# Kernel tuning notes

Hardware: AMD Instinct MI355X
Metric: run time of the kernel (lower is better)

## Reference

```python
import jax, jax.numpy as jnp
import numpy as np

NEG_BIG = -9e15  # matches torch's -9000000000000000.0 mask value
ALPHA = 0.2      # LeakyReLU negative slope


def setup_inputs() -> dict:
    key = jax.random.key(0)
    k1, k2, k3 = jax.random.split(key, 3)
    B, N, Fin, Fout = 8, 2048, 64, 64
    h = jax.random.normal(k1, (B, N, Fin), dtype=jnp.float32)
    adj = jax.random.randint(k2, (B, N, N), 0, 2, dtype=jnp.int32)
    kW, ka = jax.random.split(k3)
    # xavier_uniform with gain=1.414
    gW = 1.414 * np.sqrt(6.0 / (Fin + Fout))
    W = jax.random.uniform(kW, (Fin, Fout), minval=-gW, maxval=gW, dtype=jnp.float32)
    ga = 1.414 * np.sqrt(6.0 / (2 * Fout + 1))
    a = jax.random.uniform(ka, (2 * Fout, 1), minval=-ga, maxval=ga, dtype=jnp.float32)
    return {"h": h, "adj": adj, "W": W, "a": a}


def reference(h, adj, W, a):
    # Wh: [B, N, Fout]
    Wh = jnp.einsum("bnf,fo->bno", h, W)
    Fout = W.shape[1]
    a1 = a[:Fout, 0]   # source part of attention vector
    a2 = a[Fout:, 0]   # target part
    # e_ij = leakyrelu(a1.Wh_i + a2.Wh_j) -- rank-1 decomposition of the
    # repeat/cat construction; avoids the [B,N,N,2F] intermediate.
    s = Wh @ a1        # [B, N]
    t = Wh @ a2        # [B, N]
    e = s[:, :, None] + t[:, None, :]            # [B, N, N]
    e = jnp.where(e > 0, e, ALPHA * e)           # LeakyReLU
    e = jnp.where(adj > 0, e, NEG_BIG)           # adjacency mask
    attention = jax.nn.softmax(e, axis=2)
    # dropout omitted: reference is eval-mode (F.dropout is identity when not training)
    h_prime = jnp.einsum("bij,bjo->bio", attention, Wh)
    return jax.nn.elu(h_prime)                   # concat=True branch
```

## Files before the change

### kernel.cpp

```cpp
#include <hip/hip_runtime.h>


#define ALPHA 0.2f

typedef __attribute__((ext_vector_type(8))) short  short8;
typedef __attribute__((ext_vector_type(4))) float  f32x4;

static __device__ __forceinline__ unsigned short f2bf(float f) {
    unsigned u = __builtin_bit_cast(unsigned, f);
    u += 0x7fffu + ((u >> 16) & 1u);
    return (unsigned short)(u >> 16);
}

static __device__ __forceinline__ unsigned pack_bf2(float lo, float hi) {
    unsigned ulo = __builtin_bit_cast(unsigned, lo) + 0x8000u;
    unsigned uhi = __builtin_bit_cast(unsigned, hi) + 0x8000u;
    return __builtin_amdgcn_perm(uhi, ulo, 0x07060302);
}

__global__ __launch_bounds__(256) void k01(
    const float* __restrict__ h, const int* __restrict__ adj,
    const float* __restrict__ W, const float* __restrict__ a,
    unsigned short* __restrict__ whT, float* __restrict__ sw,
    float* __restrict__ tw, unsigned char* __restrict__ mask)
{
    __shared__ float W_l[64 * 65];
    __shared__ float wa[128];
    __shared__ float tile[4 * 16 * 65];

    const int tid = threadIdx.x;

    if (blockIdx.x >= 256) {
        const int mb = blockIdx.x - 256;
        const int4* a4 = (const int4*)adj;
        #pragma unroll 1
        for (int g0 = 0; g0 < 16; g0 += 4) {
            int4 v0a, v0b, v1a, v1b, v2a, v2b, v3a, v3b;
            const size_t p0 = (size_t)mb * 4096 + (size_t)g0 * 256 + tid;
            v0a = a4[p0 * 2];          v0b = a4[p0 * 2 + 1];
            v1a = a4[(p0 + 256) * 2];  v1b = a4[(p0 + 256) * 2 + 1];
            v2a = a4[(p0 + 512) * 2];  v2b = a4[(p0 + 512) * 2 + 1];
            v3a = a4[(p0 + 768) * 2];  v3b = a4[(p0 + 768) * 2 + 1];
            unsigned b0 = (v0a.x ? 1u:0u)|(v0a.y ? 2u:0u)|(v0a.z ? 4u:0u)|(v0a.w ? 8u:0u)
                        | (v0b.x ?16u:0u)|(v0b.y ?32u:0u)|(v0b.z ?64u:0u)|(v0b.w ?128u:0u);
            unsigned b1 = (v1a.x ? 1u:0u)|(v1a.y ? 2u:0u)|(v1a.z ? 4u:0u)|(v1a.w ? 8u:0u)
                        | (v1b.x ?16u:0u)|(v1b.y ?32u:0u)|(v1b.z ?64u:0u)|(v1b.w ?128u:0u);
            unsigned b2 = (v2a.x ? 1u:0u)|(v2a.y ? 2u:0u)|(v2a.z ? 4u:0u)|(v2a.w ? 8u:0u)
                        | (v2b.x ?16u:0u)|(v2b.y ?32u:0u)|(v2b.z ?64u:0u)|(v2b.w ?128u:0u);
            unsigned b3 = (v3a.x ? 1u:0u)|(v3a.y ? 2u:0u)|(v3a.z ? 4u:0u)|(v3a.w ? 8u:0u)
                        | (v3b.x ?16u:0u)|(v3b.y ?32u:0u)|(v3b.z ?64u:0u)|(v3b.w ?128u:0u);
            mask[p0]       = (unsigned char)b0;
            mask[p0 + 256] = (unsigned char)b1;
            mask[p0 + 512] = (unsigned char)b2;
            mask[p0 + 768] = (unsigned char)b3;
        }
        return;
    }

    const int lane = tid & 63, wv = tid >> 6;
    const int im   = lane & 15, kq = lane >> 4;

    #pragma unroll
    for (int k = 0; k < 16; ++k) {
        int e = tid + 256 * k;
        W_l[(e >> 6) * 65 + (e & 63)] = W[e];
    }
    __syncthreads();

    if (tid < 128) {
        int f = tid & 63;
        const float* ap = a + (tid >> 6) * 64;
        float acc = 0.f;
        #pragma unroll 8
        for (int o = 0; o < 64; ++o) acc += W_l[f * 65 + o] * ap[o];
        wa[tid] = acc;
    }
    __syncthreads();

    short8 bf[4][2];
    #pragma unroll
    for (int nb = 0; nb < 4; ++nb)
        #pragma unroll
        for (int ks = 0; ks < 2; ++ks)
            #pragma unroll
            for (int u = 0; u < 8; ++u)
                bf[nb][ks][u] = (short)f2bf(W_l[(ks * 32 + kq * 8 + u) * 65 + nb * 16 + im]);

    const int row0 = blockIdx.x * 64 + wv * 16;
    const int bb = row0 >> 11, n_base = row0 & 2047;
    const float* hrow = h + (size_t)(row0 + im) * 64;

    float hv[2][8];
    short8 af[2];
    float sp = 0.f, tp = 0.f;
    #pragma unroll
    for (int ks = 0; ks < 2; ++ks) {
        float4 A = *(const float4*)(hrow + ks * 32 + kq * 8);
        float4 Bv = *(const float4*)(hrow + ks * 32 + kq * 8 + 4);
        hv[ks][0] = A.x;  hv[ks][1] = A.y;  hv[ks][2] = A.z;  hv[ks][3] = A.w;
        hv[ks][4] = Bv.x; hv[ks][5] = Bv.y; hv[ks][6] = Bv.z; hv[ks][7] = Bv.w;
        #pragma unroll
        for (int u = 0; u < 8; ++u) {
            int f = ks * 32 + kq * 8 + u;
            sp += hv[ks][u] * wa[f];
            tp += hv[ks][u] * wa[64 + f];
            af[ks][u] = (short)f2bf(hv[ks][u]);
        }
    }
    sp += __shfl_xor(sp, 16, 64); sp += __shfl_xor(sp, 32, 64);
    tp += __shfl_xor(tp, 16, 64); tp += __shfl_xor(tp, 32, 64);
    if (lane < 16) {
        sw[row0 + lane] = sp;
        tw[row0 + lane] = tp;
    }

    f32x4 acc[4] = {{0.f,0.f,0.f,0.f},{0.f,0.f,0.f,0.f},{0.f,0.f,0.f,0.f},{0.f,0.f,0.f,0.f}};
    #pragma unroll
    for (int ks = 0; ks < 2; ++ks)
        #pragma unroll
        for (int nb = 0; nb < 4; ++nb)
            acc[nb] = __builtin_amdgcn_mfma_f32_16x16x32_bf16(af[ks], bf[nb][ks], acc[nb], 0, 0, 0);

    #pragma unroll
    for (int nb = 0; nb < 4; ++nb)
        #pragma unroll
        for (int r = 0; r < 4; ++r)
            tile[wv * 1040 + (kq * 4 + r) * 65 + nb * 16 + im] = acc[nb][r];
    __syncthreads();

    #pragma unroll
    for (int k = 0; k < 16; ++k) {
        int o = kq + 4 * k;
        float v = tile[wv * 1040 + im * 65 + o];
        whT[(size_t)(bb * 64 + o) * 2048 + n_base + im] = f2bf(v);
    }
}

__global__ __launch_bounds__(256, 2) void k2_attn(
    const unsigned* __restrict__ mask, const unsigned short* __restrict__ whT,
    const float* __restrict__ sw, const float* __restrict__ tw,
    float* __restrict__ out)
{
    __shared__ float t_l[2048];
    __shared__ float cpart[4 * 1040];
    __shared__ float zp[64];

    const int tid  = threadIdx.x;
    const int lane = tid & 63, wv = tid >> 6;
    const int im   = lane & 15, kq = lane >> 4;
    const int b    = blockIdx.x >> 7;
    const int i0   = (blockIdx.x & 127) << 4;

    {
        const float4* tp4 = (const float4*)(tw + (size_t)b * 2048);
        *(float4*)&t_l[tid * 4]         = tp4[tid];
        *(float4*)&t_l[(tid + 256) * 4] = tp4[tid + 256];
    }

    const uint4* mrow4 = (const uint4*)(mask + (size_t)(b * 2048 + i0 + im) * 64 + wv * 16);
    const uint4 mA = mrow4[0], mB = mrow4[1], mC = mrow4[2], mD = mrow4[3];
    const unsigned mm[16] = {mA.x, mA.y, mA.z, mA.w, mB.x, mB.y, mB.z, mB.w,
                             mC.x, mC.y, mC.z, mC.w, mD.x, mD.y, mD.z, mD.w};

    const float sl = sw[b * 2048 + i0 + im];
    const int j00 = wv * 512 + kq * 8;
    const unsigned short* whp0 = whT + ((size_t)(b * 64 +  0 + im) * 2048 + j00);
    const unsigned short* whp1 = whT + ((size_t)(b * 64 + 16 + im) * 2048 + j00);
    const unsigned short* whp2 = whT + ((size_t)(b * 64 + 32 + im) * 2048 + j00);
    const unsigned short* whp3 = whT + ((size_t)(b * 64 + 48 + im) * 2048 + j00);

    __syncthreads();

    f32x4 acc0 = {0.f,0.f,0.f,0.f}, acc1 = {0.f,0.f,0.f,0.f};
    f32x4 acc2 = {0.f,0.f,0.f,0.f}, acc3 = {0.f,0.f,0.f,0.f};
    float zs = 0.f;

    #pragma unroll
    for (int s = 0; s < 16; ++s) {
        const short8 w0 = *(const short8*)(const void*)(whp0 + s * 32);
        const short8 w1 = *(const short8*)(const void*)(whp1 + s * 32);
        const short8 w2 = *(const short8*)(const void*)(whp2 + s * 32);
        const short8 w3 = *(const short8*)(const void*)(whp3 + s * 32);

        const float4 tA = *(const float4*)&t_l[j00 + s * 32];
        const float4 tB = *(const float4*)&t_l[j00 + s * 32 + 4];
        const unsigned mbyte = (mm[s] >> (kq * 8)) & 0xffu;

        float e0 = sl + tA.x; e0 = fmaxf(e0, ALPHA * e0);
        float e1 = sl + tA.y; e1 = fmaxf(e1, ALPHA * e1);
        float e2 = sl + tA.z; e2 = fmaxf(e2, ALPHA * e2);
        float e3 = sl + tA.w; e3 = fmaxf(e3, ALPHA * e3);
        float e4 = sl + tB.x; e4 = fmaxf(e4, ALPHA * e4);
        float e5 = sl + tB.y; e5 = fmaxf(e5, ALPHA * e5);
        float e6 = sl + tB.z; e6 = fmaxf(e6, ALPHA * e6);
        float e7 = sl + tB.w; e7 = fmaxf(e7, ALPHA * e7);

        float p0 = (mbyte &   1u) ? __expf(e0) : 0.f;
        float p1 = (mbyte &   2u) ? __expf(e1) : 0.f;
        float p2 = (mbyte &   4u) ? __expf(e2) : 0.f;
        float p3 = (mbyte &   8u) ? __expf(e3) : 0.f;
        float p4 = (mbyte &  16u) ? __expf(e4) : 0.f;
        float p5 = (mbyte &  32u) ? __expf(e5) : 0.f;
        float p6 = (mbyte &  64u) ? __expf(e6) : 0.f;
        float p7 = (mbyte & 128u) ? __expf(e7) : 0.f;

        zs += ((p0 + p1) + (p2 + p3)) + ((p4 + p5) + (p6 + p7));

        int4 ai;
        ai.x = (int)pack_bf2(p0, p1);
        ai.y = (int)pack_bf2(p2, p3);
        ai.z = (int)pack_bf2(p4, p5);
        ai.w = (int)pack_bf2(p6, p7);
        const short8 af = __builtin_bit_cast(short8, ai);

        acc0 = __builtin_amdgcn_mfma_f32_16x16x32_bf16(af, w0, acc0, 0, 0, 0);
        acc1 = __builtin_amdgcn_mfma_f32_16x16x32_bf16(af, w1, acc1, 0, 0, 0);
        acc2 = __builtin_amdgcn_mfma_f32_16x16x32_bf16(af, w2, acc2, 0, 0, 0);
        acc3 = __builtin_amdgcn_mfma_f32_16x16x32_bf16(af, w3, acc3, 0, 0, 0);
    }

    zs += __shfl_xor(zs, 16, 64);
    zs += __shfl_xor(zs, 32, 64);
    if (lane < 16) zp[wv * 16 + lane] = zs;

    #pragma unroll
    for (int r = 0; r < 4; ++r) {
        cpart[wv * 1040 + (kq * 4 + r) * 65 +  0 + im] = acc0[r];
        cpart[wv * 1040 + (kq * 4 + r) * 65 + 16 + im] = acc1[r];
        cpart[wv * 1040 + (kq * 4 + r) * 65 + 32 + im] = acc2[r];
        cpart[wv * 1040 + (kq * 4 + r) * 65 + 48 + im] = acc3[r];
    }
    __syncthreads();

    #pragma unroll
    for (int k = 0; k < 4; ++k) {
        int idx = tid + 256 * k;
        int i = idx >> 6, o = idx & 63;
        float ssum = cpart[0 * 1040 + i * 65 + o] + cpart[1 * 1040 + i * 65 + o]
                   + cpart[2 * 1040 + i * 65 + o] + cpart[3 * 1040 + i * 65 + o];
        float z = zp[i] + zp[16 + i] + zp[32 + i] + zp[48 + i];
        if (z == 0.f) z = 1.f;
        float r = ssum / z;
        out[((size_t)(b * 2048 + i0 + i)) * 64 + o] = r > 0.f ? r : expm1f(r);
    }
}

extern "C" void kernel_launch(void* const* d_in, const int* in_sizes, int n_in,
                              void* d_out, int out_size, void* d_ws, size_t ws_size,
                              hipStream_t stream) {
    const float* h   = (const float*)d_in[0];
    const int*   adj = (const int*)d_in[1];
    const float* W   = (const float*)d_in[2];
    const float* a   = (const float*)d_in[3];
    float* out = (float*)d_out;

    unsigned short* whT = (unsigned short*)d_ws;
    float* sw  = (float*)((char*)d_ws + 2097152);
    float* tw  = (float*)((char*)d_ws + 2097152 + 65536);
    unsigned char* mask = (unsigned char*)((char*)d_ws + 2097152 + 131072);

    hipLaunchKernelGGL(k01, dim3(1280), dim3(256), 0, stream, h, adj, W, a, whT, sw, tw, mask);
    hipLaunchKernelGGL(k2_attn, dim3(1024), dim3(256), 0, stream,
                       (const unsigned*)mask, whT, sw, tw, out);
}
```

Baseline: 233.0 us.

## Factor exp of LeakyReLU into per-row and per-column exps; pre-swizzle Wh fragments

The attention kernel no longer evaluates exp per (i,j) pair. It precomputes exp(t_j) and exp(alpha*t_j) per column and exp(s_i), exp(alpha*s_i) per row, then forms each weight as a product, picking a branch by whether exp(s+t) exceeds one. The first kernel now writes Wh in an MFMA-fragment-ordered layout, so each lane loads one contiguous 16-byte uint4 per B operand. This removes the per-element transcendental work and the strided global loads. The cost is extra LDS traffic, and the softmax has no max subtraction, so the exp products can overflow or underflow for large s or t.

Result: faster. 214.9 us (-7.7%).

```diff
diff --git a/kernel.cpp b/kernel.cpp
--- a/kernel.cpp
+++ b/kernel.cpp
@@ -21,7 +21,7 @@
 __global__ __launch_bounds__(256) void k01(
     const float* __restrict__ h, const int* __restrict__ adj,
     const float* __restrict__ W, const float* __restrict__ a,
-    unsigned short* __restrict__ whT, float* __restrict__ sw,
+    uint4* __restrict__ whF, float* __restrict__ sw,
     float* __restrict__ tw, unsigned char* __restrict__ mask)
 {
     __shared__ float W_l[64 * 65];
@@ -87,7 +87,6 @@
                 bf[nb][ks][u] = (short)f2bf(W_l[(ks * 32 + kq * 8 + u) * 65 + nb * 16 + im]);
 
     const int row0 = blockIdx.x * 64 + wv * 16;
-    const int bb = row0 >> 11, n_base = row0 & 2047;
     const float* hrow = h + (size_t)(row0 + im) * 64;
 
     float hv[2][8];
@@ -128,20 +127,44 @@
             tile[wv * 1040 + (kq * 4 + r) * 65 + nb * 16 + im] = acc[nb][r];
     __syncthreads();
 
-    #pragma unroll
-    for (int k = 0; k < 16; ++k) {
-        int o = kq + 4 * k;
-        float v = tile[wv * 1040 + im * 65 + o];
-        whT[(size_t)(bb * 64 + o) * 2048 + n_base + im] = f2bf(v);
+    {
+        const int blk_row0 = blockIdx.x * 64;
+        const int bb2 = blk_row0 >> 11;
+        const int c_base = (blk_row0 & 2047) >> 5;
+        #pragma unroll
+        for (int k = 0; k < 2; ++k) {
+            int e = tid + 256 * k;
+            int l = e & 63, ot = (e >> 6) & 3, cl_ = e >> 8;
+            int o = ot * 16 + (l & 15);
+            int jb = cl_ * 32 + (l >> 4) * 8;
+            unsigned d0, d1, d2, d3;
+            {
+                int j0 = jb;
+                d0 = pack_bf2(tile[(j0 >> 4) * 1040 + (j0 & 15) * 65 + o],
+                              tile[(j0 >> 4) * 1040 + ((j0 & 15) + 1) * 65 + o]);
+                j0 = jb + 2;
+                d1 = pack_bf2(tile[(j0 >> 4) * 1040 + (j0 & 15) * 65 + o],
+                              tile[(j0 >> 4) * 1040 + ((j0 & 15) + 1) * 65 + o]);
+                j0 = jb + 4;
+                d2 = pack_bf2(tile[(j0 >> 4) * 1040 + (j0 & 15) * 65 + o],
+                              tile[(j0 >> 4) * 1040 + ((j0 & 15) + 1) * 65 + o]);
+                j0 = jb + 6;
+                d3 = pack_bf2(tile[(j0 >> 4) * 1040 + (j0 & 15) * 65 + o],
+                              tile[(j0 >> 4) * 1040 + ((j0 & 15) + 1) * 65 + o]);
+            }
+            uint4 val = {d0, d1, d2, d3};
+            whF[(size_t)(((bb2 * 64 + c_base + cl_) * 4 + ot)) * 64 + l] = val;
+        }
     }
 }
 
 __global__ __launch_bounds__(256, 2) void k2_attn(
-    const unsigned* __restrict__ mask, const unsigned short* __restrict__ whT,
+    const unsigned* __restrict__ mask, const uint4* __restrict__ whF,
     const float* __restrict__ sw, const float* __restrict__ tw,
     float* __restrict__ out)
 {
-    __shared__ float t_l[2048];
+    __shared__ float eB[2048];
+    __shared__ float eD[2048];
     __shared__ float cpart[4 * 1040];
     __shared__ float zp[64];
 
@@ -153,8 +176,13 @@
 
     {
         const float4* tp4 = (const float4*)(tw + (size_t)b * 2048);
-        *(float4*)&t_l[tid * 4]         = tp4[tid];
-        *(float4*)&t_l[(tid + 256) * 4] = tp4[tid + 256];
+        float4 t0 = tp4[tid], t1 = tp4[tid + 256];
+        float4 e0 = {__expf(t0.x), __expf(t0.y), __expf(t0.z), __expf(t0.w)};
+        float4 e1 = {__expf(t1.x), __expf(t1.y), __expf(t1.z), __expf(t1.w)};
+        float4 f0 = {__expf(ALPHA*t0.x), __expf(ALPHA*t0.y), __expf(ALPHA*t0.z), __expf(ALPHA*t0.w)};
+        float4 f1 = {__expf(ALPHA*t1.x), __expf(ALPHA*t1.y), __expf(ALPHA*t1.z), __expf(ALPHA*t1.w)};
+        *(float4*)&eB[tid * 4] = e0;  *(float4*)&eB[(tid + 256) * 4] = e1;
+        *(float4*)&eD[tid * 4] = f0;  *(float4*)&eD[(tid + 256) * 4] = f1;
     }
 
     const uint4* mrow4 = (const uint4*)(mask + (size_t)(b * 2048 + i0 + im) * 64 + wv * 16);
@@ -163,11 +191,9 @@
                              mC.x, mC.y, mC.z, mC.w, mD.x, mD.y, mD.z, mD.w};
 
     const float sl = sw[b * 2048 + i0 + im];
+    const float al = __expf(sl), cl_ = __expf(ALPHA * sl);
     const int j00 = wv * 512 + kq * 8;
-    const unsigned short* whp0 = whT + ((size_t)(b * 64 +  0 + im) * 2048 + j00);
-    const unsigned short* whp1 = whT + ((size_t)(b * 64 + 16 + im) * 2048 + j00);
-    const unsigned short* whp2 = whT + ((size_t)(b * 64 + 32 + im) * 2048 + j00);
-    const unsigned short* whp3 = whT + ((size_t)(b * 64 + 48 + im) * 2048 + j00);
+    const uint4* wbase = whF + (size_t)((b * 64 + wv * 16) * 4) * 64 + lane;
 
     __syncthreads();
 
@@ -177,32 +203,34 @@
 
     #pragma unroll
     for (int s = 0; s < 16; ++s) {
-        const short8 w0 = *(const short8*)(const void*)(whp0 + s * 32);
-        const short8 w1 = *(const short8*)(const void*)(whp1 + s * 32);
-        const short8 w2 = *(const short8*)(const void*)(whp2 + s * 32);
-        const short8 w3 = *(const short8*)(const void*)(whp3 + s * 32);
-
-        const float4 tA = *(const float4*)&t_l[j00 + s * 32];
-        const float4 tB = *(const float4*)&t_l[j00 + s * 32 + 4];
+        const uint4 w0 = wbase[(s * 4 + 0) * 64];
+        const uint4 w1 = wbase[(s * 4 + 1) * 64];
+        const uint4 w2 = wbase[(s * 4 + 2) * 64];
+        const uint4 w3 = wbase[(s * 4 + 3) * 64];
+
+        const float4 bA = *(const float4*)&eB[j00 + s * 32];
+        const float4 bBv = *(const float4*)&eB[j00 + s * 32 + 4];
+        const float4 dA = *(const float4*)&eD[j00 + s * 32];
+        const float4 dBv = *(const float4*)&eD[j00 + s * 32 + 4];
         const unsigned mbyte = (mm[s] >> (kq * 8)) & 0xffu;
 
-        float e0 = sl + tA.x; e0 = fmaxf(e0, ALPHA * e0);
-        float e1 = sl + tA.y; e1 = fmaxf(e1, ALPHA * e1);
-        float e2 = sl + tA.z; e2 = fmaxf(e2, ALPHA * e2);
-        float e3 = sl + tA.w; e3 = fmaxf(e3, ALPHA * e3);
-        float e4 = sl + tB.x; e4 = fmaxf(e4, ALPHA * e4);
-        float e5 = sl + tB.y; e5 = fmaxf(e5, ALPHA * e5);
-        float e6 = sl + tB.z; e6 = fmaxf(e6, ALPHA * e6);
-        float e7 = sl + tB.w; e7 = fmaxf(e7, ALPHA * e7);
-
-        float p0 = (mbyte &   1u) ? __expf(e0) : 0.f;
-        float p1 = (mbyte &   2u) ? __expf(e1) : 0.f;
-        float p2 = (mbyte &   4u) ? __expf(e2) : 0.f;
-        float p3 = (mbyte &   8u) ? __expf(e3) : 0.f;
-        float p4 = (mbyte &  16u) ? __expf(e4) : 0.f;
-        float p5 = (mbyte &  32u) ? __expf(e5) : 0.f;
-        float p6 = (mbyte &  64u) ? __expf(e6) : 0.f;
-        float p7 = (mbyte & 128u) ? __expf(e7) : 0.f;
+        float m0 = al * bA.x, n0 = cl_ * dA.x;
+        float m1 = al * bA.y, n1 = cl_ * dA.y;
+        float m2 = al * bA.z, n2 = cl_ * dA.z;
+        float m3 = al * bA.w, n3 = cl_ * dA.w;
+        float m4 = al * bBv.x, n4 = cl_ * dBv.x;
+        float m5 = al * bBv.y, n5 = cl_ * dBv.y;
+        float m6 = al * bBv.z, n6 = cl_ * dBv.z;
+        float m7 = al * bBv.w, n7 = cl_ * dBv.w;
+
+        float p0 = m0 > 1.f ? m0 : n0;  p0 = (mbyte &   1u) ? p0 : 0.f;
+        float p1 = m1 > 1.f ? m1 : n1;  p1 = (mbyte &   2u) ? p1 : 0.f;
+        float p2 = m2 > 1.f ? m2 : n2;  p2 = (mbyte &   4u) ? p2 : 0.f;
+        float p3 = m3 > 1.f ? m3 : n3;  p3 = (mbyte &   8u) ? p3 : 0.f;
+        float p4 = m4 > 1.f ? m4 : n4;  p4 = (mbyte &  16u) ? p4 : 0.f;
+        float p5 = m5 > 1.f ? m5 : n5;  p5 = (mbyte &  32u) ? p5 : 0.f;
+        float p6 = m6 > 1.f ? m6 : n6;  p6 = (mbyte &  64u) ? p6 : 0.f;
+        float p7 = m7 > 1.f ? m7 : n7;  p7 = (mbyte & 128u) ? p7 : 0.f;
 
         zs += ((p0 + p1) + (p2 + p3)) + ((p4 + p5) + (p6 + p7));
 
@@ -213,10 +241,10 @@
         ai.w = (int)pack_bf2(p6, p7);
         const short8 af = __builtin_bit_cast(short8, ai);
 
-        acc0 = __builtin_amdgcn_mfma_f32_16x16x32_bf16(af, w0, acc0, 0, 0, 0);
-        acc1 = __builtin_amdgcn_mfma_f32_16x16x32_bf16(af, w1, acc1, 0, 0, 0);
-        acc2 = __builtin_amdgcn_mfma_f32_16x16x32_bf16(af, w2, acc2, 0, 0, 0);
-        acc3 = __builtin_amdgcn_mfma_f32_16x16x32_bf16(af, w3, acc3, 0, 0, 0);
+        acc0 = __builtin_amdgcn_mfma_f32_16x16x32_bf16(af, __builtin_bit_cast(short8, w0), acc0, 0, 0, 0);
+        acc1 = __builtin_amdgcn_mfma_f32_16x16x32_bf16(af, __builtin_bit_cast(short8, w1), acc1, 0, 0, 0);
+        acc2 = __builtin_amdgcn_mfma_f32_16x16x32_bf16(af, __builtin_bit_cast(short8, w2), acc2, 0, 0, 0);
+        acc3 = __builtin_amdgcn_mfma_f32_16x16x32_bf16(af, __builtin_bit_cast(short8, w3), acc3, 0, 0, 0);
     }
 
     zs += __shfl_xor(zs, 16, 64);
@@ -254,12 +282,12 @@
     const float* a   = (const float*)d_in[3];
     float* out = (float*)d_out;
 
-    unsigned short* whT = (unsigned short*)d_ws;
+    uint4* whF = (uint4*)d_ws;
     float* sw  = (float*)((char*)d_ws + 2097152);
     float* tw  = (float*)((char*)d_ws + 2097152 + 65536);
     unsigned char* mask = (unsigned char*)((char*)d_ws + 2097152 + 131072);
 
-    hipLaunchKernelGGL(k01, dim3(1280), dim3(256), 0, stream, h, adj, W, a, whT, sw, tw, mask);
+    hipLaunchKernelGGL(k01, dim3(1280), dim3(256), 0, stream, h, adj, W, a, whF, sw, tw, mask);
     hipLaunchKernelGGL(k2_attn, dim3(1024), dim3(256), 0, stream,
-                       (const unsigned*)mask, whT, sw, tw, out);
-}
+                       (const unsigned*)mask, whF, sw, tw, out);
+}
```
